# Kernel optimization log

Hardware: AMD Instinct MI355X
Metric: run time of the kernel (lower is better)

The kernel has to match this reference:

```python
import jax, jax.numpy as jnp
from jax import lax
import numpy as np

K = 4          # kernel_size
DEPTH = 2      # sig_depth
B, S, CIN = 64, 1024, 5
H1, H2 = 64, 16
OUT = 32
C1 = H2 + CIN + 1            # channels entering signature1 (include_original + include_time)
SIG_C1 = C1 + C1 * C1        # 506
SIG_C2 = H2 + H2 * H2        # 272


def setup_inputs() -> dict:
    key = jax.random.key(0)
    ks = jax.random.split(key, 12)
    def w(k, shape, fan_in):
        return jax.random.normal(k, shape, jnp.float32) * (1.0 / np.sqrt(fan_in))
    inp = {}
    inp["x"] = jax.random.normal(ks[0], (B, S, CIN), jnp.float32)
    inp["lengths"] = jax.random.randint(ks[1], (B,), S // 2, S + 1)
    # Augment 1: Conv1d(CIN->H1, k=K), Conv1d(H1->H1, 1), Conv1d(H1->H2, 1)
    inp["a1_w0"] = w(ks[2], (H1, CIN, K), CIN * K); inp["a1_b0"] = jnp.zeros((H1,), jnp.float32)
    inp["a1_w1"] = w(ks[3], (H1, H1, 1), H1);       inp["a1_b1"] = jnp.zeros((H1,), jnp.float32)
    inp["a1_w2"] = w(ks[4], (H2, H1, 1), H1);       inp["a1_b2"] = jnp.zeros((H2,), jnp.float32)
    # Augment 2: Conv1d(SIG_C1->H1, k=K), Conv1d(H1->H1, 1), Conv1d(H1->H2, 1)
    inp["a2_w0"] = w(ks[5], (H1, SIG_C1, K), SIG_C1 * K); inp["a2_b0"] = jnp.zeros((H1,), jnp.float32)
    inp["a2_w1"] = w(ks[6], (H1, H1, 1), H1);             inp["a2_b1"] = jnp.zeros((H1,), jnp.float32)
    inp["a2_w2"] = w(ks[7], (H2, H1, 1), H1);             inp["a2_b2"] = jnp.zeros((H2,), jnp.float32)
    inp["lin_w"] = w(ks[8], (OUT, SIG_C2), SIG_C2)
    inp["lin_b"] = jnp.zeros((OUT,), jnp.float32)
    return inp


def _conv1d(x, w, b):
    # x: (B, C, L), w: (O, I, k) -> (B, O, L-k+1), VALID (no padding), stride 1
    y = lax.conv_general_dilated(x, w, (1,), 'VALID', dimension_numbers=('NCH', 'OIH', 'NCH'))
    return y + b[None, :, None]


def _augment(x, ws, bs, kernel_size, include_original, include_time):
    # signatory.Augment: relu between convs, none after last; concat [original_trunc, time, conv_out]
    b_, s_, _ = x.shape
    L = s_ - kernel_size + 1
    pieces = []
    if include_original:
        pieces.append(x[:, kernel_size - 1:, :])
    if include_time:
        t = jnp.linspace(0.0, 1.0, L, dtype=x.dtype)
        pieces.append(jnp.broadcast_to(t[None, :, None], (b_, L, 1)))
    h = jnp.swapaxes(x, 1, 2)
    h = _conv1d(h, ws[0], bs[0])
    for wi, bi in zip(ws[1:], bs[1:]):
        h = _conv1d(jax.nn.relu(h), wi, bi)
    pieces.append(jnp.swapaxes(h, 1, 2))
    return jnp.concatenate(pieces, axis=2)


def _sig_exp(dx, depth):
    # tensor-algebra exp of a linear segment: level k = dx^{\otimes k} / k!
    levels = [dx]
    cur = dx
    for k in range(2, depth + 1):
        cur = (cur[..., :, None] * dx[..., None, :]).reshape(dx.shape[:-1] + (-1,)) / k
        levels.append(cur)
    return levels


def _chen(a, b, depth):
    # Chen's relation: (a*b)_k = a_k + sum_{i=1}^{k-1} a_i (x) b_{k-i} + b_k
    out = []
    for k in range(1, depth + 1):
        acc = a[k - 1] + b[k - 1]
        for i in range(1, k):
            acc = acc + (a[i - 1][:, :, None] * b[k - i - 1][:, None, :]).reshape(acc.shape)
        out.append(acc)
    return tuple(out)


def _signature(x, depth, stream):
    # basepoint=True: prepend zero point, so increments are diff with zero prepended
    b_, s_, c_ = x.shape
    dx = jnp.diff(x, axis=1, prepend=jnp.zeros((b_, 1, c_), x.dtype))
    exps = tuple(jnp.moveaxis(e, 1, 0) for e in _sig_exp(dx, depth))  # each (S, B, c^k)
    init = tuple(jnp.zeros((b_, c_ ** k), x.dtype) for k in range(1, depth + 1))  # identity (levels=0)
    def step(carry, e):
        new = _chen(carry, e, depth)
        return new, (new if stream else None)
    carry, ys = lax.scan(step, init, exps)
    if stream:
        return jnp.concatenate([jnp.moveaxis(y, 0, 1) for y in ys], axis=2)
    return jnp.concatenate(carry, axis=1)


def _become_constant(x, lengths):
    # y[i,j] = x[i,j] if j < lengths[i] else x[i, lengths[i]-1]
    b_, s_, _ = x.shape
    idx = jnp.minimum(jnp.arange(s_)[None, :], (lengths - 1)[:, None])
    return x[jnp.arange(b_)[:, None], idx]


def reference(x, lengths, a1_w0, a1_b0, a1_w1, a1_b1, a1_w2, a1_b2,
              a2_w0, a2_b0, a2_w1, a2_b1, a2_w2, a2_b2, lin_w, lin_b):
    h = _augment(x, (a1_w0, a1_w1, a1_w2), (a1_b0, a1_b1, a1_b2), K, True, True)   # (B, S-K+1, C1)
    s1 = _signature(h, DEPTH, True)                                                # (B, S-K+1, SIG_C1)
    h2 = _augment(s1, (a2_w0, a2_w1, a2_w2), (a2_b0, a2_b1, a2_b2), K, False, False)  # (B, S-2K+2, H2)
    adj = lengths - 2 * K + 2
    h2 = _become_constant(h2, adj)
    s2 = _signature(h2, DEPTH, False)                                              # (B, SIG_C2)
    return s2 @ lin_w.T + lin_b
```

## Files before the change

kernel.cpp:

```cpp
#include <hip/hip_runtime.h>
#include <hip/hip_bf16.h>

#define B_    64
#define S_    1024
#define CIN   5
#define K_    4
#define H1    64
#define H2    16
#define OUT_  32
#define L1_   1021
#define C1    22
#define C1SQ  484
#define SIGC1 506
#define L2_   1018
#define SIGC2 272
#define NCH   32
#define CH1   32

typedef __attribute__((ext_vector_type(8))) short short8;
typedef __attribute__((ext_vector_type(16))) float f32x16;

__device__ __forceinline__ unsigned short f2bf(float v) {
  __hip_bfloat16 h = __float2bfloat16(v);
  return *reinterpret_cast<unsigned short*>(&h);
}
__device__ __forceinline__ float bf2f(unsigned short u) {
  __hip_bfloat16 h;
  *reinterpret_cast<unsigned short*>(&h) = u;
  return __bfloat162float(h);
}

__global__ __launch_bounds__(256) void aug1_kernel(
    const float* __restrict__ x,
    const float* __restrict__ w0, const float* __restrict__ b0,
    const float* __restrict__ w1, const float* __restrict__ b1,
    const float* __restrict__ w2, const float* __restrict__ b2,
    float* __restrict__ h) {
  int b = blockIdx.y;
  int l = blockIdx.x * 256 + threadIdx.x;
  if (l >= L1_) return;
  const float* xb = x + (size_t)b * S_ * CIN;

  float t1[H1];
#pragma unroll
  for (int o = 0; o < H1; ++o) t1[o] = b0[o];
  for (int j = 0; j < K_; ++j) {
    for (int c = 0; c < CIN; ++c) {
      float xv = xb[(l + j) * CIN + c];
#pragma unroll
      for (int o = 0; o < H1; ++o) t1[o] += xv * w0[o * (CIN * K_) + c * K_ + j];
    }
  }
#pragma unroll
  for (int o = 0; o < H1; ++o) t1[o] = fmaxf(t1[o], 0.f);

  float t3[H2];
#pragma unroll
  for (int q = 0; q < H2; ++q) t3[q] = b2[q];
  for (int ch = 0; ch < 4; ++ch) {
    float t2c[16];
    for (int oc = 0; oc < 16; ++oc) {
      int o = ch * 16 + oc;
      float a = b1[o];
#pragma unroll
      for (int i = 0; i < H1; ++i) a += t1[i] * w1[o * H1 + i];
      t2c[oc] = fmaxf(a, 0.f);
    }
#pragma unroll
    for (int q = 0; q < H2; ++q) {
      float a = t3[q];
#pragma unroll
      for (int oc = 0; oc < 16; ++oc) a += t2c[oc] * w2[q * H1 + ch * 16 + oc];
      t3[q] = a;
    }
  }

  float* hr = h + ((size_t)b * L1_ + l) * C1;
#pragma unroll
  for (int c = 0; c < CIN; ++c) hr[c] = xb[(l + K_ - 1) * CIN + c];
  hr[CIN] = (float)l / (float)(L1_ - 1);
#pragma unroll
  for (int q = 0; q < H2; ++q) hr[CIN + 1 + q] = t3[q];
}

__global__ __launch_bounds__(512) void sig1a_kernel(const float* __restrict__ h, float* __restrict__ tot1) {
  int kt = blockIdx.x, b = blockIdx.y;
  int tid = threadIdx.x;
  if (tid >= C1SQ) return;
  int start = kt * 256;
  const float* hb = h + (size_t)b * L1_ * C1;
  int i = tid / C1, j = tid - i * C1;
  float hpi = 0.f, hpj = 0.f;
  if (kt > 0) {
    hpi = hb[(start - 1) * C1 + i];
    hpj = hb[(start - 1) * C1 + j];
  }
  float pi = 0.f, pj = 0.f, s2 = 0.f;
  for (int t = start; t < start + 256; ++t) {
    float ci = hb[t * C1 + i] - hpi;
    float cj = hb[t * C1 + j] - hpj;
    float dj = cj - pj;
    s2 += pi * dj + 0.5f * (ci - pi) * dj;
    pi = ci;
    pj = cj;
  }
  tot1[((size_t)b * 4 + kt) * C1SQ + tid] = s2;
}

__global__ __launch_bounds__(256) void wt2_kernel(const float* __restrict__ w0,
                                                  unsigned short* __restrict__ bhi,
                                                  unsigned short* __restrict__ blo) {
  int idx = blockIdx.x * 256 + threadIdx.x;
  if (idx >= 2 * 128 * 64 * 8) return;
  int e = idx & 7;
  int lane = (idx >> 3) & 63;
  int ksg = (idx >> 9) & 127;
  int ot = idx >> 16;
  int j = ksg >> 5, cc = (ksg >> 2) & 7, ks = ksg & 3;
  int o = ot * 32 + (lane & 31);
  int c = cc * 64 + ks * 16 + (lane >> 5) * 8 + e;
  float v = (c < SIGC1) ? w0[o * (SIGC1 * K_) + c * K_ + j] : 0.f;
  unsigned short hb16 = f2bf(v);
  bhi[idx] = hb16;
  blo[idx] = f2bf(v - bf2f(hb16));
}

__global__ __launch_bounds__(512) void conv2pw_kernel(
    const float* __restrict__ h, const float* __restrict__ tot1,
    const unsigned short* __restrict__ bpkhi, const unsigned short* __restrict__ bpklo,
    const float* __restrict__ b0,
    const float* __restrict__ w1, const float* __restrict__ b1,
    const float* __restrict__ w2, const float* __restrict__ b2,
    float* __restrict__ h2) {
  __shared__ __align__(16) char smem[160768];
  int tid = threadIdx.x;
  int lane = tid & 63, w = tid >> 6;
  int wm = w >> 1, wo = w & 1;
  int k = blockIdx.x, b = blockIdx.y, l0 = k * 256;
  const float* hb = h + (size_t)b * L1_ * C1;
  const char* bhg = (const char*)bpkhi;
  const char* blg = (const char*)bpklo;
  float* hs = (float*)smem;
  char* Ah = smem + 23552;
  char* Al = smem + 57344;
  char* Bs = smem + 91136;
  float* gsum = (float*)(smem + 156672);
  float* s2pl = (float*)(smem + 158720);

  for (int idx = tid; idx < 265 * C1; idx += 512) {
    int r = idx / C1, c = idx - r * C1;
    float v = 0.f;
    if (!(k == 0 && r == 0)) {
      int hr = l0 - 1 + r;
      if (hr > L1_ - 1) hr = L1_ - 1;
      v = hb[hr * C1 + c];
    }
    hs[idx] = v;
  }
  if (tid < C1SQ) {
    int i = tid / C1, j = tid - i * C1;
    float s2pv = 0.f;
    for (int kp = 0; kp < k; ++kp) {
      float bvi = 0.f, bvj = 0.f;
      if (kp > 0) {
        bvi = hb[(256 * kp - 1) * C1 + i];
        bvj = hb[(256 * kp - 1) * C1 + j];
      }
      float bv1j = hb[(256 * (kp + 1) - 1) * C1 + j];
      s2pv += bvi * (bv1j - bvj) + tot1[((size_t)b * 4 + kp) * C1SQ + tid];
    }
    s2pl[tid] = s2pv;
  }
  __syncthreads();

  f32x16 a0HH = {}, a0HL = {}, a0LH = {}, a1HH = {}, a1HL = {}, a1LH = {};
  int khalf = lane >> 5;
  int r0 = 64 * wm + (lane & 31);

  for (int cc = 0; cc < 8; ++cc) {
    if (cc) __syncthreads();
    for (int s = w; s < 64; s += 8) {
      int p = s >> 2, ot = (s >> 1) & 1, plane = s & 1;
      int jj = p >> 2, ks = p & 3;
      int ksg = jj * 32 + cc * 4 + ks;
      const char* src = (plane ? blg : bhg) + (size_t)(ot * 128 + ksg) * 1024 + lane * 16;
      __builtin_amdgcn_global_load_lds(
          (const __attribute__((address_space(1))) void*)src,
          (__attribute__((address_space(3))) void*)(Bs + ((p * 2 + ot) * 2 + plane) * 1024), 16, 0, 0);
    }
    int c = cc * 64 + lane;
    bool isS2 = (c >= C1 && c < SIGC1);
    int ii = 0, jj2 = 0;
    if (isS2) {
      int idx = c - C1;
      ii = idx / C1;
      jj2 = idx - ii * C1;
    }
    float hpi = hs[ii], hpj = hs[jj2];
    int u0 = w * 33;
    {
      float pi = hs[u0 * C1 + ii] - hpi;
      float pj = hs[u0 * C1 + jj2] - hpj;
      float loc = 0.f;
#pragma unroll 3
      for (int s = 0; s < 33; ++s) {
        int u = u0 + s;
        float ci = hs[(u + 1) * C1 + ii] - hpi;
        float cj = hs[(u + 1) * C1 + jj2] - hpj;
        float dj = cj - pj;
        loc += pi * dj + 0.5f * (ci - pi) * dj;
        pi = ci;
        pj = cj;
      }
      gsum[w * 64 + lane] = loc;
    }
    __syncthreads();
    {
      float s2r = isS2 ? s2pl[c - C1] : 0.f;
      for (int gp = 0; gp < w; ++gp) s2r += gsum[gp * 64 + lane];
      float pi = hs[u0 * C1 + ii] - hpi;
      float pj = hs[u0 * C1 + jj2] - hpj;
#pragma unroll 3
      for (int s = 0; s < 33; ++s) {
        int u = u0 + s;
        float v;
        if (isS2) {
          float ci = hs[(u + 1) * C1 + ii] - hpi;
          float cj = hs[(u + 1) * C1 + jj2] - hpj;
          float dj = cj - pj;
          s2r += pi * dj + 0.5f * (ci - pi) * dj;
          pi = ci;
          pj = cj;
          v = s2r + hpi * cj;
        } else if (c < C1) {
          v = hs[(u + 1) * C1 + c];
        } else {
          v = 0.f;
        }
        unsigned short hb16 = f2bf(v);
        unsigned short lb16 = f2bf(v - bf2f(hb16));
        int boff = u * 128 + ((((lane >> 3) ^ (u & 7))) << 4) + (lane & 7) * 2;
        *(unsigned short*)(Ah + boff) = hb16;
        *(unsigned short*)(Al + boff) = lb16;
      }
    }
    __syncthreads();
#pragma unroll
    for (int j = 0; j < 4; ++j) {
      int ra0 = r0 + j, ra1 = ra0 + 32;
      int rx0 = ra0 & 7, rx1 = ra1 & 7;
      const char* a0b = Ah + ra0 * 128;
      const char* a0bl = Al + ra0 * 128;
      const char* a1b = Ah + ra1 * 128;
      const char* a1bl = Al + ra1 * 128;
#pragma unroll
      for (int ks = 0; ks < 4; ++ks) {
        int p = j * 4 + ks;
        const char* bb = Bs + (size_t)((p * 2 + wo) * 2) * 1024 + lane * 16;
        short8 b_h = *(const short8*)bb;
        short8 b_l = *(const short8*)(bb + 1024);
        int g0 = ((ks * 2 + khalf) ^ rx0) << 4;
        int g1 = ((ks * 2 + khalf) ^ rx1) << 4;
        short8 v0h = *(const short8*)(a0b + g0);
        short8 v0l = *(const short8*)(a0bl + g0);
        short8 v1h = *(const short8*)(a1b + g1);
        short8 v1l = *(const short8*)(a1bl + g1);
        a0HH = __builtin_amdgcn_mfma_f32_32x32x16_bf16(v0h, b_h, a0HH, 0, 0, 0);
        a0HL = __builtin_amdgcn_mfma_f32_32x32x16_bf16(v0h, b_l, a0HL, 0, 0, 0);
        a0LH = __builtin_amdgcn_mfma_f32_32x32x16_bf16(v0l, b_h, a0LH, 0, 0, 0);
        a1HH = __builtin_amdgcn_mfma_f32_32x32x16_bf16(v1h, b_h, a1HH, 0, 0, 0);
        a1HL = __builtin_amdgcn_mfma_f32_32x32x16_bf16(v1h, b_l, a1HL, 0, 0, 0);
        a1LH = __builtin_amdgcn_mfma_f32_32x32x16_bf16(v1l, b_h, a1LH, 0, 0, 0);
      }
    }
  }
  __syncthreads();
  float* t1s = (float*)smem;
  float* t2s = (float*)(smem + 66560);
  float* wl = (float*)(smem + 133120);
  for (int i2 = tid; i2 < 4096; i2 += 512) wl[i2] = w1[i2];
  for (int i2 = tid; i2 < 1024; i2 += 512) wl[4096 + i2] = w2[i2];
  {
    int col = 32 * wo + (lane & 31);
    float bbv = b0[col];
    int rbase = 64 * wm + 4 * (lane >> 5);
#pragma unroll
    for (int rg = 0; rg < 16; ++rg) {
      int row = (rg & 3) + 8 * (rg >> 2) + rbase;
      t1s[row * 65 + col] = fmaxf(a0HH[rg] + a0HL[rg] + a0LH[rg] + bbv, 0.f);
      t1s[(row + 32) * 65 + col] = fmaxf(a1HH[rg] + a1HL[rg] + a1LH[rg] + bbv, 0.f);
    }
  }
  __syncthreads();
  {
    int row = tid & 255, qh = tid >> 8;
    float tr[64];
#pragma unroll
    for (int i2 = 0; i2 < 64; ++i2) tr[i2] = t1s[row * 65 + i2];
#pragma unroll
    for (int oc = 0; oc < 32; ++oc) {
      int o = qh * 32 + oc;
      float a = b1[o];
      const float4* wr = (const float4*)(wl + o * 64);
#pragma unroll
      for (int i4 = 0; i4 < 16; ++i4) {
        float4 wv = wr[i4];
        a += tr[i4 * 4] * wv.x + tr[i4 * 4 + 1] * wv.y +
             tr[i4 * 4 + 2] * wv.z + tr[i4 * 4 + 3] * wv.w;
      }
      t2s[row * 65 + o] = fmaxf(a, 0.f);
    }
  }
  __syncthreads();
  {
    int row = tid & 255, ph = tid >> 8;
    int l = l0 + row;
    if (l < L2_) {
      float tr2[64];
#pragma unroll
      for (int i2 = 0; i2 < 64; ++i2) tr2[i2] = t2s[row * 65 + i2];
      float* outr = h2 + ((size_t)b * L2_ + l) * H2;
#pragma unroll
      for (int pp = 0; pp < 8; ++pp) {
        int pch = ph * 8 + pp;
        float a = b2[pch];
        const float4* wr = (const float4*)(wl + 4096 + pch * 64);
#pragma unroll
        for (int i4 = 0; i4 < 16; ++i4) {
          float4 wv = wr[i4];
          a += tr2[i4 * 4] * wv.x + tr2[i4 * 4 + 1] * wv.y +
               tr2[i4 * 4 + 2] * wv.z + tr2[i4 * 4 + 3] * wv.w;
        }
        outr[pch] = a;
      }
    }
  }
}

__global__ __launch_bounds__(256) void sig2a_kernel(const float* __restrict__ h2, const int* __restrict__ lengths,
                                                    float* __restrict__ s2tot2) {
  int k = blockIdx.x, b = blockIdx.y;
  int tid = threadIdx.x;
  int i = tid >> 4, j = tid & 15;
  int adjm1 = lengths[b] - (2 * K_ - 2) - 1;
  int start = k * CH1, end = min(start + CH1 - 1, L2_ - 1);
  size_t oidx = ((size_t)b * NCH + k) * 256 + tid;
  if (k > 0 && start - 1 >= adjm1) {
    s2tot2[oidx] = 0.f;
    return;
  }
  const float* h2b = h2 + (size_t)b * L2_ * H2;
  float hpi = 0.f, hpj = 0.f;
  if (k > 0) {
    int row = min(start - 1, adjm1);
    hpi = h2b[row * H2 + i];
    hpj = h2b[row * H2 + j];
  }
  float pi = 0.f, pj = 0.f, s2 = 0.f;
  for (int t = start; t <= end; ++t) {
    int row = min(t, adjm1);
    float ci = h2b[row * H2 + i] - hpi;
    float cj = h2b[row * H2 + j] - hpj;
    float dj = cj - pj;
    s2 += pi * dj + 0.5f * (ci - pi) * dj;
    pi = ci;
    pj = cj;
  }
  s2tot2[oidx] = s2;
}

__global__ __launch_bounds__(256) void sig2b_kernel(const float* __restrict__ h2, const int* __restrict__ lengths,
                                                    const float* __restrict__ s2tot2,
                                                    const float* __restrict__ lin_w, const float* __restrict__ lin_b,
                                                    float* __restrict__ out) {
  int b = blockIdx.x;
  int tid = threadIdx.x;
  int i = tid >> 4, j = tid & 15;
  int adjm1 = lengths[b] - (2 * K_ - 2) - 1;
  const float* h2b = h2 + (size_t)b * L2_ * H2;
  __shared__ float bv[NCH + 1][H2];
  __shared__ float s2s[SIGC2];
  for (int idx = tid; idx < (NCH + 1) * H2; idx += 256) {
    int kk = idx >> 4, c = idx & 15;
    float v = 0.f;
    if (kk > 0) {
      int row = min(min(CH1 * kk - 1, L2_ - 1), adjm1);
      v = h2b[row * H2 + c];
    }
    bv[kk][c] = v;
  }
  __syncthreads();
  float s2 = 0.f;
  for (int k = 0; k < NCH; ++k) {
    s2 += bv[k][i] * (bv[k + 1][j] - bv[k][j]) + s2tot2[((size_t)b * NCH + k) * 256 + tid];
  }
  s2s[H2 + tid] = s2;
  if (tid < H2) s2s[tid] = bv[NCH][tid];
  __syncthreads();
  if (tid < OUT_) {
    float a = lin_b[tid];
    for (int c = 0; c < SIGC2; ++c) a += s2s[c] * lin_w[tid * SIGC2 + c];
    out[b * OUT_ + tid] = a;
  }
}

extern "C" void kernel_launch(void* const* d_in, const int* in_sizes, int n_in,
                              void* d_out, int out_size, void* d_ws, size_t ws_size,
                              hipStream_t stream) {
  const float* x      = (const float*)d_in[0];
  const int*   lengths= (const int*)d_in[1];
  const float* a1_w0  = (const float*)d_in[2];
  const float* a1_b0  = (const float*)d_in[3];
  const float* a1_w1  = (const float*)d_in[4];
  const float* a1_b1  = (const float*)d_in[5];
  const float* a1_w2  = (const float*)d_in[6];
  const float* a1_b2  = (const float*)d_in[7];
  const float* a2_w0  = (const float*)d_in[8];
  const float* a2_b0  = (const float*)d_in[9];
  const float* a2_w1  = (const float*)d_in[10];
  const float* a2_b1  = (const float*)d_in[11];
  const float* a2_w2  = (const float*)d_in[12];
  const float* a2_b2  = (const float*)d_in[13];
  const float* lin_w  = (const float*)d_in[14];
  const float* lin_b  = (const float*)d_in[15];
  float* outp = (float*)d_out;

  float* ws = (float*)d_ws;
  float* h = ws;
  unsigned short* bpkhi = (unsigned short*)(ws + 1437568);
  unsigned short* bpklo = bpkhi + 131072;
  float* h2 = ws + 1568640;
  float* tot1 = ws + 2611072;
  float* s2tot2 = ws + 2734976;

  aug1_kernel<<<dim3(4, B_), 256, 0, stream>>>(x, a1_w0, a1_b0, a1_w1, a1_b1, a1_w2, a1_b2, h);
  wt2_kernel<<<(2 * 128 * 64 * 8 + 255) / 256, 256, 0, stream>>>(a2_w0, bpkhi, bpklo);
  sig1a_kernel<<<dim3(3, B_), 512, 0, stream>>>(h, tot1);
  conv2pw_kernel<<<dim3(4, B_), 512, 0, stream>>>(h, tot1, bpkhi, bpklo, a2_b0,
                                                  a2_w1, a2_b1, a2_w2, a2_b2, h2);
  sig2a_kernel<<<dim3(NCH, B_), 256, 0, stream>>>(h2, lengths, s2tot2);
  sig2b_kernel<<<B_, 256, 0, stream>>>(h2, lengths, s2tot2, lin_w, lin_b, outp);
}
```

Measured before the change: 265.0 us.

## Halve conv2 row tile to 128 and double-buffer A tiles in LDS

Shrinks the per-block row tile of the fused signature+conv2 kernel from 256 to 128 positions, doubling the grid to 8x64 blocks and the sig1a prefix chunks to 7. Each wave now computes one 32-row MFMA tile instead of two, and the A operand buffers are double-buffered across channel chunks. The pointwise stages are remapped to four threads per row. The goal is more parallelism and better CU occupancy, at the cost of more redundant prefix work (longer kp loop) and halo loads per block.

```diff
diff --git a/kernel.cpp b/kernel.cpp
--- a/kernel.cpp
+++ b/kernel.cpp
@@ -87,7 +87,7 @@
   int kt = blockIdx.x, b = blockIdx.y;
   int tid = threadIdx.x;
   if (tid >= C1SQ) return;
-  int start = kt * 256;
+  int start = kt * 128;
   const float* hb = h + (size_t)b * L1_ * C1;
   int i = tid / C1, j = tid - i * C1;
   float hpi = 0.f, hpj = 0.f;
@@ -96,7 +96,8 @@
     hpj = hb[(start - 1) * C1 + j];
   }
   float pi = 0.f, pj = 0.f, s2 = 0.f;
-  for (int t = start; t < start + 256; ++t) {
+#pragma unroll 4
+  for (int t = start; t < start + 128; ++t) {
     float ci = hb[t * C1 + i] - hpi;
     float cj = hb[t * C1 + j] - hpj;
     float dj = cj - pj;
@@ -104,7 +105,7 @@
     pi = ci;
     pj = cj;
   }
-  tot1[((size_t)b * 4 + kt) * C1SQ + tid] = s2;
+  tot1[((size_t)b * 8 + kt) * C1SQ + tid] = s2;
 }
 
 __global__ __launch_bounds__(256) void wt2_kernel(const float* __restrict__ w0,
@@ -132,22 +133,21 @@
     const float* __restrict__ w1, const float* __restrict__ b1,
     const float* __restrict__ w2, const float* __restrict__ b2,
     float* __restrict__ h2) {
-  __shared__ __align__(16) char smem[160768];
+  __shared__ __align__(16) char smem[151552];
   int tid = threadIdx.x;
   int lane = tid & 63, w = tid >> 6;
   int wm = w >> 1, wo = w & 1;
-  int k = blockIdx.x, b = blockIdx.y, l0 = k * 256;
+  int k = blockIdx.x, b = blockIdx.y, l0 = k * 128;
   const float* hb = h + (size_t)b * L1_ * C1;
   const char* bhg = (const char*)bpkhi;
   const char* blg = (const char*)bpklo;
   float* hs = (float*)smem;
-  char* Ah = smem + 23552;
-  char* Al = smem + 57344;
-  char* Bs = smem + 91136;
-  float* gsum = (float*)(smem + 156672);
-  float* s2pl = (float*)(smem + 158720);
-
-  for (int idx = tid; idx < 265 * C1; idx += 512) {
+  char* Abuf = smem + 12288;
+  char* Bs = smem + 81920;
+  float* gsum = (float*)(smem + 147456);
+  float* s2pl = (float*)(smem + 149504);
+
+  for (int idx = tid; idx < 137 * C1; idx += 512) {
     int r = idx / C1, c = idx - r * C1;
     float v = 0.f;
     if (!(k == 0 && r == 0)) {
@@ -163,19 +163,19 @@
     for (int kp = 0; kp < k; ++kp) {
       float bvi = 0.f, bvj = 0.f;
       if (kp > 0) {
-        bvi = hb[(256 * kp - 1) * C1 + i];
-        bvj = hb[(256 * kp - 1) * C1 + j];
-      }
-      float bv1j = hb[(256 * (kp + 1) - 1) * C1 + j];
-      s2pv += bvi * (bv1j - bvj) + tot1[((size_t)b * 4 + kp) * C1SQ + tid];
+        bvi = hb[(128 * kp - 1) * C1 + i];
+        bvj = hb[(128 * kp - 1) * C1 + j];
+      }
+      float bv1j = hb[(128 * (kp + 1) - 1) * C1 + j];
+      s2pv += bvi * (bv1j - bvj) + tot1[((size_t)b * 8 + kp) * C1SQ + tid];
     }
     s2pl[tid] = s2pv;
   }
   __syncthreads();
 
-  f32x16 a0HH = {}, a0HL = {}, a0LH = {}, a1HH = {}, a1HL = {}, a1LH = {};
+  f32x16 aHH = {}, aHL = {}, aLH = {};
   int khalf = lane >> 5;
-  int r0 = 64 * wm + (lane & 31);
+  int r0 = 32 * wm + (lane & 31);
 
   for (int cc = 0; cc < 8; ++cc) {
     if (cc) __syncthreads();
@@ -188,6 +188,8 @@
           (const __attribute__((address_space(1))) void*)src,
           (__attribute__((address_space(3))) void*)(Bs + ((p * 2 + ot) * 2 + plane) * 1024), 16, 0, 0);
     }
+    char* Ah = Abuf + (cc & 1) * 34816;
+    char* Al = Ah + 17408;
     int c = cc * 64 + lane;
     bool isS2 = (c >= C1 && c < SIGC1);
     int ii = 0, jj2 = 0;
@@ -197,13 +199,12 @@
       jj2 = idx - ii * C1;
     }
     float hpi = hs[ii], hpj = hs[jj2];
-    int u0 = w * 33;
+    int u0 = w * 17;
     {
       float pi = hs[u0 * C1 + ii] - hpi;
       float pj = hs[u0 * C1 + jj2] - hpj;
       float loc = 0.f;
-#pragma unroll 3
-      for (int s = 0; s < 33; ++s) {
+      for (int s = 0; s < 17; ++s) {
         int u = u0 + s;
         float ci = hs[(u + 1) * C1 + ii] - hpi;
         float cj = hs[(u + 1) * C1 + jj2] - hpj;
@@ -220,8 +221,7 @@
       for (int gp = 0; gp < w; ++gp) s2r += gsum[gp * 64 + lane];
       float pi = hs[u0 * C1 + ii] - hpi;
       float pj = hs[u0 * C1 + jj2] - hpj;
-#pragma unroll 3
-      for (int s = 0; s < 33; ++s) {
+      for (int s = 0; s < 17; ++s) {
         int u = u0 + s;
         float v;
         if (isS2) {
@@ -239,7 +239,7 @@
         }
         unsigned short hb16 = f2bf(v);
         unsigned short lb16 = f2bf(v - bf2f(hb16));
-        int boff = u * 128 + ((((lane >> 3) ^ (u & 7))) << 4) + (lane & 7) * 2;
+        int boff = u * 128 + (((lane >> 3) ^ (u & 7)) << 4) + (lane & 7) * 2;
         *(unsigned short*)(Ah + boff) = hb16;
         *(unsigned short*)(Al + boff) = lb16;
       }
@@ -247,59 +247,51 @@
     __syncthreads();
 #pragma unroll
     for (int j = 0; j < 4; ++j) {
-      int ra0 = r0 + j, ra1 = ra0 + 32;
-      int rx0 = ra0 & 7, rx1 = ra1 & 7;
-      const char* a0b = Ah + ra0 * 128;
-      const char* a0bl = Al + ra0 * 128;
-      const char* a1b = Ah + ra1 * 128;
-      const char* a1bl = Al + ra1 * 128;
+      int ra = r0 + j;
+      int rx = ra & 7;
+      const char* ab = Ah + ra * 128;
+      const char* abl = Al + ra * 128;
 #pragma unroll
       for (int ks = 0; ks < 4; ++ks) {
         int p = j * 4 + ks;
         const char* bb = Bs + (size_t)((p * 2 + wo) * 2) * 1024 + lane * 16;
         short8 b_h = *(const short8*)bb;
         short8 b_l = *(const short8*)(bb + 1024);
-        int g0 = ((ks * 2 + khalf) ^ rx0) << 4;
-        int g1 = ((ks * 2 + khalf) ^ rx1) << 4;
-        short8 v0h = *(const short8*)(a0b + g0);
-        short8 v0l = *(const short8*)(a0bl + g0);
-        short8 v1h = *(const short8*)(a1b + g1);
-        short8 v1l = *(const short8*)(a1bl + g1);
-        a0HH = __builtin_amdgcn_mfma_f32_32x32x16_bf16(v0h, b_h, a0HH, 0, 0, 0);
-        a0HL = __builtin_amdgcn_mfma_f32_32x32x16_bf16(v0h, b_l, a0HL, 0, 0, 0);
-        a0LH = __builtin_amdgcn_mfma_f32_32x32x16_bf16(v0l, b_h, a0LH, 0, 0, 0);
-        a1HH = __builtin_amdgcn_mfma_f32_32x32x16_bf16(v1h, b_h, a1HH, 0, 0, 0);
-        a1HL = __builtin_amdgcn_mfma_f32_32x32x16_bf16(v1h, b_l, a1HL, 0, 0, 0);
-        a1LH = __builtin_amdgcn_mfma_f32_32x32x16_bf16(v1l, b_h, a1LH, 0, 0, 0);
+        int g0 = ((ks * 2 + khalf) ^ rx) << 4;
+        short8 vh = *(const short8*)(ab + g0);
+        short8 vl = *(const short8*)(abl + g0);
+        aHH = __builtin_amdgcn_mfma_f32_32x32x16_bf16(vh, b_h, aHH, 0, 0, 0);
+        aHL = __builtin_amdgcn_mfma_f32_32x32x16_bf16(vh, b_l, aHL, 0, 0, 0);
+        aLH = __builtin_amdgcn_mfma_f32_32x32x16_bf16(vl, b_h, aLH, 0, 0, 0);
       }
     }
   }
   __syncthreads();
   float* t1s = (float*)smem;
-  float* t2s = (float*)(smem + 66560);
-  float* wl = (float*)(smem + 133120);
+  float* t2s = (float*)(smem + 33280);
+  float* wl = (float*)(smem + 66560);
   for (int i2 = tid; i2 < 4096; i2 += 512) wl[i2] = w1[i2];
   for (int i2 = tid; i2 < 1024; i2 += 512) wl[4096 + i2] = w2[i2];
   {
     int col = 32 * wo + (lane & 31);
     float bbv = b0[col];
-    int rbase = 64 * wm + 4 * (lane >> 5);
+    int rbase = 32 * wm + 4 * khalf;
 #pragma unroll
     for (int rg = 0; rg < 16; ++rg) {
       int row = (rg & 3) + 8 * (rg >> 2) + rbase;
-      t1s[row * 65 + col] = fmaxf(a0HH[rg] + a0HL[rg] + a0LH[rg] + bbv, 0.f);
-      t1s[(row + 32) * 65 + col] = fmaxf(a1HH[rg] + a1HL[rg] + a1LH[rg] + bbv, 0.f);
+      t1s[row * 65 + col] = fmaxf(aHH[rg] + aHL[rg] + aLH[rg] + bbv, 0.f);
     }
   }
   __syncthreads();
   {
-    int row = tid & 255, qh = tid >> 8;
+    int row = tid >> 2, q = tid & 3;
+    const float* trow = t1s + row * 65;
     float tr[64];
 #pragma unroll
-    for (int i2 = 0; i2 < 64; ++i2) tr[i2] = t1s[row * 65 + i2];
-#pragma unroll
-    for (int oc = 0; oc < 32; ++oc) {
-      int o = qh * 32 + oc;
+    for (int i2 = 0; i2 < 64; ++i2) tr[i2] = trow[i2];
+#pragma unroll
+    for (int oc = 0; oc < 16; ++oc) {
+      int o = q * 16 + oc;
       float a = b1[o];
       const float4* wr = (const float4*)(wl + o * 64);
 #pragma unroll
@@ -313,16 +305,17 @@
   }
   __syncthreads();
   {
-    int row = tid & 255, ph = tid >> 8;
+    int row = tid >> 2, pg = tid & 3;
     int l = l0 + row;
     if (l < L2_) {
+      const float* trow = t2s + row * 65;
       float tr2[64];
 #pragma unroll
-      for (int i2 = 0; i2 < 64; ++i2) tr2[i2] = t2s[row * 65 + i2];
+      for (int i2 = 0; i2 < 64; ++i2) tr2[i2] = trow[i2];
       float* outr = h2 + ((size_t)b * L2_ + l) * H2;
 #pragma unroll
-      for (int pp = 0; pp < 8; ++pp) {
-        int pch = ph * 8 + pp;
+      for (int pp = 0; pp < 4; ++pp) {
+        int pch = pg * 4 + pp;
         float a = b2[pch];
         const float4* wr = (const float4*)(wl + 4096 + pch * 64);
 #pragma unroll
@@ -357,6 +350,7 @@
     hpj = h2b[row * H2 + j];
   }
   float pi = 0.f, pj = 0.f, s2 = 0.f;
+#pragma unroll 4
   for (int t = start; t <= end; ++t) {
     int row = min(t, adjm1);
     float ci = h2b[row * H2 + i] - hpi;
@@ -431,12 +425,12 @@
   unsigned short* bpklo = bpkhi + 131072;
   float* h2 = ws + 1568640;
   float* tot1 = ws + 2611072;
-  float* s2tot2 = ws + 2734976;
+  float* s2tot2 = ws + 2858880;
 
   aug1_kernel<<<dim3(4, B_), 256, 0, stream>>>(x, a1_w0, a1_b0, a1_w1, a1_b1, a1_w2, a1_b2, h);
   wt2_kernel<<<(2 * 128 * 64 * 8 + 255) / 256, 256, 0, stream>>>(a2_w0, bpkhi, bpklo);
-  sig1a_kernel<<<dim3(3, B_), 512, 0, stream>>>(h, tot1);
-  conv2pw_kernel<<<dim3(4, B_), 512, 0, stream>>>(h, tot1, bpkhi, bpklo, a2_b0,
+  sig1a_kernel<<<dim3(7, B_), 512, 0, stream>>>(h, tot1);
+  conv2pw_kernel<<<dim3(8, B_), 512, 0, stream>>>(h, tot1, bpkhi, bpklo, a2_b0,
                                                   a2_w1, a2_b1, a2_w2, a2_b2, h2);
   sig2a_kernel<<<dim3(NCH, B_), 256, 0, stream>>>(h2, lengths, s2tot2);
   sig2b_kernel<<<B_, 256, 0, stream>>>(h2, lengths, s2tot2, lin_w, lin_b, outp);
```

Result: slower. 290.2 us (+9.5%).
